# Optimization experiments

Hardware: AMD Instinct MI355X
Metric: run time of the kernel (lower is better)

## Reference

```python
import jax, jax.numpy as jnp
import numpy as np

N, K, D = 32768, 8192, 64

def setup_inputs() -> dict:
    key = jax.random.key(0)
    kx, kc = jax.random.split(key)
    x = jax.random.normal(kx, (N, D), dtype=jnp.float32)
    codebook = jax.random.normal(kc, (K, D), dtype=jnp.float32)
    return {"x": x, "codebook": codebook}

def reference(x, codebook):
    # Faithful to: argmin(((codebook[None] - x[:, None])**2).sum(-1), -1)
    # Computed via the expanded squared distance to avoid the [N, K, D]
    # constant per row and does not affect argmin, but we include it so the
    # distance matrix matches the original math exactly.
    x_sq = jnp.sum(x * x, axis=-1, keepdims=True)          # [N, 1]
    c_sq = jnp.sum(codebook * codebook, axis=-1)           # [K]
    cross = jnp.einsum('nd,kd->nk', x, codebook)           # [N, K]
    dists = x_sq - 2.0 * cross + c_sq[None, :]             # [N, K]
    return jnp.argmin(dists, axis=-1)                      # [N] int32
```

## Files before the change

kernel.cpp:

```cpp
#include <hip/hip_runtime.h>
#include <math.h>


typedef __attribute__((ext_vector_type(8)))  _Float16 h8v;
typedef __attribute__((ext_vector_type(16))) float f16v;
typedef __attribute__((ext_vector_type(4)))  float f4v;

constexpr int NROWS = 32768;
constexpr int KC    = 8192;
constexpr int DD    = 64;
constexpr int TPB   = 256;
constexpr int BROWS = 64;
constexpr int BTILE = 64;
constexpr int NT    = KC / BTILE;
constexpr int TILE_HALFS = BTILE * DD * 2;

__device__ __forceinline__ void split2h(float v, _Float16& h1, _Float16& h2) {
  const float av = fabsf(v);
  _Float16 a = (_Float16)v;
  if (av < 6.1035156e-5f) a = (_Float16)0.f;
  h1 = a;
  h2 = (_Float16)((v - (float)a) * 4096.f);
}

__device__ __forceinline__ void gload_lds16(const void* g, void* l) {
  __builtin_amdgcn_global_load_lds(
      (const __attribute__((address_space(1))) void*)g,
      (__attribute__((address_space(3))) void*)l, 16, 0, 0);
}

__global__ void vq_pre_kernel(const float* __restrict__ x,
                              const float* __restrict__ cb,
                              _Float16* __restrict__ bSwz,
                              float* __restrict__ csq,
                              float* __restrict__ xsq) {
  const int bid = blockIdx.x, tid = threadIdx.x;
  if (bid < KC / TPB) {
    const int code = bid * TPB + tid;
    const float* cp = cb + (size_t)code * DD;
    float v[DD];
#pragma unroll
    for (int d = 0; d < DD; d += 4) {
      const float4 g = *(const float4*)(cp + d);
      v[d] = g.x; v[d + 1] = g.y; v[d + 2] = g.z; v[d + 3] = g.w;
    }
    float s = 0.f;
#pragma unroll
    for (int d = 0; d < DD; ++d) s = fmaf(v[d], v[d], s);
    csq[code] = s;
    _Float16 p1[DD], p2[DD];
#pragma unroll
    for (int d = 0; d < DD; ++d) split2h(v[d], p1[d], p2[d]);
    const int g = code >> 5, l = code & 31;
    _Float16* base = bSwz + (size_t)g * 4096;
#pragma unroll
    for (int p = 0; p < 2; ++p) {
      const _Float16* pl = p ? p2 : p1;
#pragma unroll
      for (int kc4 = 0; kc4 < 4; ++kc4)
#pragma unroll
        for (int h = 0; h < 2; ++h) {
          h8v wv;
#pragma unroll
          for (int j = 0; j < 8; ++j) wv[j] = pl[kc4 * 16 + h * 8 + j];
          *(h8v*)(base + (p * 4 + kc4) * 512 + (h * 32 + l) * 8) = wv;
        }
    }
  } else {
    const int n = (bid - KC / TPB) * TPB + tid;
    const float* xp = x + (size_t)n * DD;
    float s = 0.f;
#pragma unroll
    for (int d = 0; d < DD; ++d) s = fmaf(xp[d], xp[d], s);
    xsq[n] = s;
  }
}

__global__ __launch_bounds__(TPB, 2)
void vq_mfma_kernel(const float* __restrict__ x, const _Float16* __restrict__ bSwz,
                    const float* __restrict__ csq_g, const float* __restrict__ xsq_g,
                    int* __restrict__ out) {
  __shared__ alignas(16) _Float16 ldsA[2][BROWS][DD];
  __shared__ alignas(16) _Float16 ldsB[2][TILE_HALFS];
  __shared__ alignas(16) float ldsXsq[BROWS];
  __shared__ unsigned long long ldsRed[BROWS][2];

  const int tid  = threadIdx.x;
  const int lane = tid & 63;
  const int w    = tid >> 6;
  const int s    = w & 1;
  const int ch   = w >> 1;
  const int half = lane >> 5;
  const int col  = lane & 31;
  const int blockRow = blockIdx.x * BROWS;

  {
    const _Float16* src0 = bSwz + (size_t)(w * 4) * 512 + lane * 8;
#pragma unroll
    for (int j = 0; j < 4; ++j)
      gload_lds16(src0 + j * 512, &ldsB[0][(w * 4 + j) * 512]);
  }
  {
    const int row = tid >> 2, dseg = (tid & 3) * 16;
    const float* xp = x + (size_t)(blockRow + row) * DD + dseg;
    float v[16];
#pragma unroll
    for (int d = 0; d < 16; d += 4) {
      const float4 g = *(const float4*)(xp + d);
      v[d] = g.x; v[d + 1] = g.y; v[d + 2] = g.z; v[d + 3] = g.w;
    }
    _Float16 qa[16], qb[16];
#pragma unroll
    for (int e = 0; e < 16; ++e) split2h(v[e], qa[e], qb[e]);
#pragma unroll
    for (int h2 = 0; h2 < 2; ++h2) {
      h8v a, b;
#pragma unroll
      for (int j = 0; j < 8; ++j) { a[j] = qa[h2 * 8 + j]; b[j] = qb[h2 * 8 + j]; }
      *(h8v*)&ldsA[0][row][dseg + h2 * 8] = a;
      *(h8v*)&ldsA[1][row][dseg + h2 * 8] = b;
    }
  }
  if (tid < BROWS) ldsXsq[tid] = xsq_g[blockRow + tid];
  __syncthreads();

  h8v afr[2][4];
#pragma unroll
  for (int p = 0; p < 2; ++p)
#pragma unroll
    for (int kc4 = 0; kc4 < 4; ++kc4)
      afr[p][kc4] = *(const h8v*)&ldsA[p][s * 32 + col][kc4 * 16 + half * 8];

  float xq[16];
  {
    const float* xb = &ldsXsq[s * 32 + 4 * half];
#pragma unroll
    for (int g8 = 0; g8 < 4; ++g8) {
      const f4v t4 = *(const f4v*)(xb + g8 * 8);
      xq[g8 * 4] = t4[0]; xq[g8 * 4 + 1] = t4[1];
      xq[g8 * 4 + 2] = t4[2]; xq[g8 * 4 + 3] = t4[3];
    }
  }

  float bestD[16];
  unsigned bestC[16];
#pragma unroll
  for (int i = 0; i < 16; ++i) { bestD[i] = INFINITY; bestC[i] = 0u; }

  for (int t = 0; t < NT; ++t) {
    const int buf = t & 1;
    if (t + 1 < NT) {
      const _Float16* src =
          bSwz + (size_t)(t + 1) * TILE_HALFS + (size_t)(w * 4) * 512 + lane * 8;
#pragma unroll
      for (int j = 0; j < 4; ++j)
        gload_lds16(src + j * 512, &ldsB[buf ^ 1][(w * 4 + j) * 512]);
    }
    const float cs = csq_g[t * BTILE + ch * 32 + col];

    h8v bfr[2][4];
#pragma unroll
    for (int p = 0; p < 2; ++p)
#pragma unroll
      for (int kc4 = 0; kc4 < 4; ++kc4)
        bfr[p][kc4] = *(const h8v*)
            &ldsB[buf][(ch * 8 + p * 4 + kc4) * 512 + lane * 8];

    f16v accA  = {0.f,0.f,0.f,0.f,0.f,0.f,0.f,0.f,0.f,0.f,0.f,0.f,0.f,0.f,0.f,0.f};
    f16v accB1 = {0.f,0.f,0.f,0.f,0.f,0.f,0.f,0.f,0.f,0.f,0.f,0.f,0.f,0.f,0.f,0.f};
    f16v accB2 = {0.f,0.f,0.f,0.f,0.f,0.f,0.f,0.f,0.f,0.f,0.f,0.f,0.f,0.f,0.f,0.f};
#pragma unroll
    for (int kc4 = 0; kc4 < 4; ++kc4) {
      accA  = __builtin_amdgcn_mfma_f32_32x32x16_f16(afr[0][kc4], bfr[0][kc4], accA,  0, 0, 0);
      accB1 = __builtin_amdgcn_mfma_f32_32x32x16_f16(afr[0][kc4], bfr[1][kc4], accB1, 0, 0, 0);
      accB2 = __builtin_amdgcn_mfma_f32_32x32x16_f16(afr[1][kc4], bfr[0][kc4], accB2, 0, 0, 0);
    }

    const unsigned code = (unsigned)(t * BTILE + ch * 32 + col);
#pragma unroll
    for (int i = 0; i < 16; ++i) {
      const float acc = fmaf(accB1[i] + accB2[i], 2.44140625e-4f, accA[i]);
      const float dist = fmaf(-2.f, acc, xq[i]) + cs;
      if (dist < bestD[i]) { bestD[i] = dist; bestC[i] = code; }
    }
    __syncthreads();
  }

  unsigned long long key[16];
#pragma unroll
  for (int i = 0; i < 16; ++i)
    key[i] = ((unsigned long long)__float_as_uint(bestD[i]) << 32) | bestC[i];
#pragma unroll
  for (int i = 0; i < 16; ++i) {
#pragma unroll
    for (int m = 1; m < 32; m <<= 1) {
      const unsigned long long o = __shfl_xor(key[i], m, 64);
      if (o < key[i]) key[i] = o;
    }
  }
  if (col == 0) {
#pragma unroll
    for (int i = 0; i < 16; ++i) {
      const int row = s * 32 + (i & 3) + 8 * (i >> 2) + 4 * half;
      ldsRed[row][ch] = key[i];
    }
  }
  __syncthreads();
  if (tid < BROWS) {
    const unsigned long long a = ldsRed[tid][0];
    const unsigned long long b = ldsRed[tid][1];
    out[blockRow + tid] = (int)(unsigned)((a < b ? a : b) & 0xFFFFFFFFull);
  }
}

extern "C" void kernel_launch(void* const* d_in, const int* in_sizes, int n_in,
                              void* d_out, int out_size, void* d_ws, size_t ws_size,
                              hipStream_t stream) {
  const float* x  = (const float*)d_in[0];
  const float* cb = (const float*)d_in[1];
  int* out = (int*)d_out;

  _Float16* bSwz = (_Float16*)d_ws;
  float* csq_g = (float*)((char*)d_ws + (size_t)KC * DD * 2 * 2);
  float* xsq_g = csq_g + KC;

  vq_pre_kernel<<<dim3(KC / TPB + NROWS / TPB), dim3(TPB), 0, stream>>>(
      x, cb, bSwz, csq_g, xsq_g);
  vq_mfma_kernel<<<dim3(NROWS / BROWS), dim3(TPB), 0, stream>>>(
      x, bSwz, csq_g, xsq_g, out);
}
```

Measured before the change: 192.6 us.

## Triple-buffer codebook tiles with software-pipelined MFMA epilogue and fused x-norm

The main loop moves to a three-buffer LDS ring that prefetches two tiles ahead. Codebook norms are staged into LDS alongside each tile, and synchronisation uses a raw waitcnt+barrier that allows outstanding loads to remain in flight. Each tile's argmin epilogue is deferred so it overlaps the next tile's MFMAs, and the two correction MFMAs share one accumulator. The x-norm computation moves from the pre-kernel into the main kernel, shrinking the pre-kernel, at the cost of more LDS, more registers, and fragile hand-counted vmcnt values.

```diff
diff --git a/kernel.cpp b/kernel.cpp
--- a/kernel.cpp
+++ b/kernel.cpp
@@ -14,6 +14,7 @@
 constexpr int BTILE = 64;
 constexpr int NT    = KC / BTILE;
 constexpr int TILE_HALFS = BTILE * DD * 2;
+constexpr int BUF_HALFS  = TILE_HALFS + 512;
 
 __device__ __forceinline__ void split2h(float v, _Float16& h1, _Float16& h2) {
   const float av = fabsf(v);
@@ -28,60 +29,96 @@
       (const __attribute__((address_space(1))) void*)g,
       (__attribute__((address_space(3))) void*)l, 16, 0, 0);
 }
-
-__global__ void vq_pre_kernel(const float* __restrict__ x,
-                              const float* __restrict__ cb,
+__device__ __forceinline__ void gload_lds4(const void* g, void* l) {
+  __builtin_amdgcn_global_load_lds(
+      (const __attribute__((address_space(1))) void*)g,
+      (__attribute__((address_space(3))) void*)l, 4, 0, 0);
+}
+
+__global__ void vq_pre_kernel(const float* __restrict__ cb,
                               _Float16* __restrict__ bSwz,
-                              float* __restrict__ csq,
-                              float* __restrict__ xsq) {
+                              float* __restrict__ csq) {
   const int bid = blockIdx.x, tid = threadIdx.x;
-  if (bid < KC / TPB) {
-    const int code = bid * TPB + tid;
-    const float* cp = cb + (size_t)code * DD;
-    float v[DD];
-#pragma unroll
-    for (int d = 0; d < DD; d += 4) {
-      const float4 g = *(const float4*)(cp + d);
-      v[d] = g.x; v[d + 1] = g.y; v[d + 2] = g.z; v[d + 3] = g.w;
-    }
-    float s = 0.f;
-#pragma unroll
-    for (int d = 0; d < DD; ++d) s = fmaf(v[d], v[d], s);
-    csq[code] = s;
-    _Float16 p1[DD], p2[DD];
-#pragma unroll
-    for (int d = 0; d < DD; ++d) split2h(v[d], p1[d], p2[d]);
-    const int g = code >> 5, l = code & 31;
-    _Float16* base = bSwz + (size_t)g * 4096;
-#pragma unroll
-    for (int p = 0; p < 2; ++p) {
-      const _Float16* pl = p ? p2 : p1;
-#pragma unroll
-      for (int kc4 = 0; kc4 < 4; ++kc4)
-#pragma unroll
-        for (int h = 0; h < 2; ++h) {
-          h8v wv;
-#pragma unroll
-          for (int j = 0; j < 8; ++j) wv[j] = pl[kc4 * 16 + h * 8 + j];
-          *(h8v*)(base + (p * 4 + kc4) * 512 + (h * 32 + l) * 8) = wv;
-        }
-    }
-  } else {
-    const int n = (bid - KC / TPB) * TPB + tid;
-    const float* xp = x + (size_t)n * DD;
-    float s = 0.f;
-#pragma unroll
-    for (int d = 0; d < DD; ++d) s = fmaf(xp[d], xp[d], s);
-    xsq[n] = s;
-  }
-}
+  const int code = bid * TPB + tid;
+  const float* cp = cb + (size_t)code * DD;
+  float v[DD];
+#pragma unroll
+  for (int d = 0; d < DD; d += 4) {
+    const float4 g = *(const float4*)(cp + d);
+    v[d] = g.x; v[d + 1] = g.y; v[d + 2] = g.z; v[d + 3] = g.w;
+  }
+  float s = 0.f;
+#pragma unroll
+  for (int d = 0; d < DD; ++d) s = fmaf(v[d], v[d], s);
+  csq[code] = s;
+  _Float16 p1[DD], p2[DD];
+#pragma unroll
+  for (int d = 0; d < DD; ++d) split2h(v[d], p1[d], p2[d]);
+  const int g = code >> 5, l = code & 31;
+  _Float16* base = bSwz + (size_t)g * 4096;
+#pragma unroll
+  for (int p = 0; p < 2; ++p) {
+    const _Float16* pl = p ? p2 : p1;
+#pragma unroll
+    for (int kc4 = 0; kc4 < 4; ++kc4)
+#pragma unroll
+      for (int h = 0; h < 2; ++h) {
+        h8v wv;
+#pragma unroll
+        for (int j = 0; j < 8; ++j) wv[j] = pl[kc4 * 16 + h * 8 + j];
+        *(h8v*)(base + (p * 4 + kc4) * 512 + (h * 32 + l) * 8) = wv;
+      }
+  }
+}
+
+#define TILE_BODY(T, BUFC, PFB, AA, AB, CS, CODE, PA, PB, PCS, PCODE, DOEPI, DOISSUE, WN) \
+  {                                                                                       \
+    _Float16* bp = ldsBf + (BUFC) * BUF_HALFS;                                            \
+    h8v b0[4], b1[4];                                                                     \
+    {                                                                                     \
+      const _Float16* rb = bp + (ch * 8) * 512 + lane * 8;                                \
+      _Pragma("unroll")                                                                   \
+      for (int kc = 0; kc < 4; ++kc) {                                                    \
+        b0[kc] = *(const h8v*)(rb + kc * 512);                                            \
+        b1[kc] = *(const h8v*)(rb + (4 + kc) * 512);                                      \
+      }                                                                                   \
+    }                                                                                     \
+    CS = ((const float*)(bp + TILE_HALFS))[w * 64 + wcode];                               \
+    CODE = (unsigned)((T) * 64) + wcode;                                                  \
+    if (DOISSUE) {                                                                        \
+      const _Float16* gs = bSwz + (size_t)((T) + 2) * TILE_HALFS + (w * 4) * 512 + lane * 8; \
+      _Float16* ld = ldsBf + (PFB) * BUF_HALFS;                                           \
+      _Pragma("unroll")                                                                   \
+      for (int j = 0; j < 4; ++j)                                                         \
+        gload_lds16(gs + j * 512, ld + (w * 4 + j) * 512);                                \
+      gload_lds4(csq_g + ((T) + 2) * 64 + lane, (float*)(ld + TILE_HALFS) + w * 64);      \
+    }                                                                                     \
+    AA = __builtin_amdgcn_mfma_f32_32x32x16_f16(afr[0][0], b0[0], Zacc, 0, 0, 0);         \
+    AB = __builtin_amdgcn_mfma_f32_32x32x16_f16(afr[0][0], b1[0], Zacc, 0, 0, 0);         \
+    _Pragma("unroll")                                                                     \
+    for (int kc = 1; kc < 4; ++kc) {                                                      \
+      AA = __builtin_amdgcn_mfma_f32_32x32x16_f16(afr[0][kc], b0[kc], AA, 0, 0, 0);       \
+      AB = __builtin_amdgcn_mfma_f32_32x32x16_f16(afr[0][kc], b1[kc], AB, 0, 0, 0);       \
+    }                                                                                     \
+    _Pragma("unroll")                                                                     \
+    for (int kc = 0; kc < 4; ++kc)                                                        \
+      AB = __builtin_amdgcn_mfma_f32_32x32x16_f16(afr[1][kc], b0[kc], AB, 0, 0, 0);       \
+    if (DOEPI) {                                                                          \
+      _Pragma("unroll")                                                                   \
+      for (int i = 0; i < 16; ++i) {                                                      \
+        const float a_ = fmaf(PB[i], 2.44140625e-4f, PA[i]);                              \
+        const float d_ = fmaf(-2.f, a_, xq[i]) + PCS;                                     \
+        if (d_ < bestD[i]) { bestD[i] = d_; bestC[i] = PCODE; }                           \
+      }                                                                                   \
+    }                                                                                     \
+    asm volatile("s_waitcnt vmcnt(" #WN ") lgkmcnt(0)\n\ts_barrier" ::: "memory");        \
+  }
 
 __global__ __launch_bounds__(TPB, 2)
 void vq_mfma_kernel(const float* __restrict__ x, const _Float16* __restrict__ bSwz,
-                    const float* __restrict__ csq_g, const float* __restrict__ xsq_g,
-                    int* __restrict__ out) {
+                    const float* __restrict__ csq_g, int* __restrict__ out) {
   __shared__ alignas(16) _Float16 ldsA[2][BROWS][DD];
-  __shared__ alignas(16) _Float16 ldsB[2][TILE_HALFS];
+  __shared__ alignas(16) _Float16 ldsBf[3 * BUF_HALFS];
   __shared__ alignas(16) float ldsXsq[BROWS];
   __shared__ unsigned long long ldsRed[BROWS][2];
 
@@ -92,13 +129,17 @@
   const int ch   = w >> 1;
   const int half = lane >> 5;
   const int col  = lane & 31;
+  const int wcode = ch * 32 + col;
   const int blockRow = blockIdx.x * BROWS;
 
-  {
-    const _Float16* src0 = bSwz + (size_t)(w * 4) * 512 + lane * 8;
+#pragma unroll
+  for (int tt = 0; tt < 2; ++tt) {
+    const _Float16* gs = bSwz + (size_t)tt * TILE_HALFS + (w * 4) * 512 + lane * 8;
+    _Float16* ld = ldsBf + tt * BUF_HALFS;
 #pragma unroll
     for (int j = 0; j < 4; ++j)
-      gload_lds16(src0 + j * 512, &ldsB[0][(w * 4 + j) * 512]);
+      gload_lds16(gs + j * 512, ld + (w * 4 + j) * 512);
+    gload_lds4(csq_g + tt * 64 + lane, (float*)(ld + TILE_HALFS) + w * 64);
   }
   {
     const int row = tid >> 2, dseg = (tid & 3) * 16;
@@ -109,6 +150,12 @@
       const float4 g = *(const float4*)(xp + d);
       v[d] = g.x; v[d + 1] = g.y; v[d + 2] = g.z; v[d + 3] = g.w;
     }
+    float p = 0.f;
+#pragma unroll
+    for (int e = 0; e < 16; ++e) p = fmaf(v[e], v[e], p);
+    p += __shfl_xor(p, 1, 64);
+    p += __shfl_xor(p, 2, 64);
+    if ((tid & 3) == 0) ldsXsq[row] = p;
     _Float16 qa[16], qb[16];
 #pragma unroll
     for (int e = 0; e < 16; ++e) split2h(v[e], qa[e], qb[e]);
@@ -121,7 +168,6 @@
       *(h8v*)&ldsA[1][row][dseg + h2 * 8] = b;
     }
   }
-  if (tid < BROWS) ldsXsq[tid] = xsq_g[blockRow + tid];
   __syncthreads();
 
   h8v afr[2][4];
@@ -147,43 +193,32 @@
 #pragma unroll
   for (int i = 0; i < 16; ++i) { bestD[i] = INFINITY; bestC[i] = 0u; }
 
-  for (int t = 0; t < NT; ++t) {
-    const int buf = t & 1;
-    if (t + 1 < NT) {
-      const _Float16* src =
-          bSwz + (size_t)(t + 1) * TILE_HALFS + (size_t)(w * 4) * 512 + lane * 8;
-#pragma unroll
-      for (int j = 0; j < 4; ++j)
-        gload_lds16(src + j * 512, &ldsB[buf ^ 1][(w * 4 + j) * 512]);
-    }
-    const float cs = csq_g[t * BTILE + ch * 32 + col];
-
-    h8v bfr[2][4];
-#pragma unroll
-    for (int p = 0; p < 2; ++p)
-#pragma unroll
-      for (int kc4 = 0; kc4 < 4; ++kc4)
-        bfr[p][kc4] = *(const h8v*)
-            &ldsB[buf][(ch * 8 + p * 4 + kc4) * 512 + lane * 8];
-
-    f16v accA  = {0.f,0.f,0.f,0.f,0.f,0.f,0.f,0.f,0.f,0.f,0.f,0.f,0.f,0.f,0.f,0.f};
-    f16v accB1 = {0.f,0.f,0.f,0.f,0.f,0.f,0.f,0.f,0.f,0.f,0.f,0.f,0.f,0.f,0.f,0.f};
-    f16v accB2 = {0.f,0.f,0.f,0.f,0.f,0.f,0.f,0.f,0.f,0.f,0.f,0.f,0.f,0.f,0.f,0.f};
-#pragma unroll
-    for (int kc4 = 0; kc4 < 4; ++kc4) {
-      accA  = __builtin_amdgcn_mfma_f32_32x32x16_f16(afr[0][kc4], bfr[0][kc4], accA,  0, 0, 0);
-      accB1 = __builtin_amdgcn_mfma_f32_32x32x16_f16(afr[0][kc4], bfr[1][kc4], accB1, 0, 0, 0);
-      accB2 = __builtin_amdgcn_mfma_f32_32x32x16_f16(afr[1][kc4], bfr[0][kc4], accB2, 0, 0, 0);
-    }
-
-    const unsigned code = (unsigned)(t * BTILE + ch * 32 + col);
-#pragma unroll
-    for (int i = 0; i < 16; ++i) {
-      const float acc = fmaf(accB1[i] + accB2[i], 2.44140625e-4f, accA[i]);
-      const float dist = fmaf(-2.f, acc, xq[i]) + cs;
-      if (dist < bestD[i]) { bestD[i] = dist; bestC[i] = code; }
-    }
-    __syncthreads();
+  const f16v Zacc = {0.f,0.f,0.f,0.f,0.f,0.f,0.f,0.f,0.f,0.f,0.f,0.f,0.f,0.f,0.f,0.f};
+  f16v aA0 = Zacc, aB0 = Zacc, aA1 = Zacc, aB1 = Zacc;
+  float cs0 = 0.f, cs1 = 0.f;
+  unsigned code0 = 0u, code1 = 0u;
+
+  TILE_BODY(0, 0, 2, aA0, aB0, cs0, code0, aA1, aB1, cs1, code1, false, true, 5);
+  TILE_BODY(1, 1, 0, aA1, aB1, cs1, code1, aA0, aB0, cs0, code0, true,  true, 5);
+  for (int t = 2; t < 122; t += 6) {
+    TILE_BODY(t,     2, 1, aA0, aB0, cs0, code0, aA1, aB1, cs1, code1, true, true, 5);
+    TILE_BODY(t + 1, 0, 2, aA1, aB1, cs1, code1, aA0, aB0, cs0, code0, true, true, 5);
+    TILE_BODY(t + 2, 1, 0, aA0, aB0, cs0, code0, aA1, aB1, cs1, code1, true, true, 5);
+    TILE_BODY(t + 3, 2, 1, aA1, aB1, cs1, code1, aA0, aB0, cs0, code0, true, true, 5);
+    TILE_BODY(t + 4, 0, 2, aA0, aB0, cs0, code0, aA1, aB1, cs1, code1, true, true, 5);
+    TILE_BODY(t + 5, 1, 0, aA1, aB1, cs1, code1, aA0, aB0, cs0, code0, true, true, 5);
+  }
+  TILE_BODY(122, 2, 1, aA0, aB0, cs0, code0, aA1, aB1, cs1, code1, true, true,  5);
+  TILE_BODY(123, 0, 2, aA1, aB1, cs1, code1, aA0, aB0, cs0, code0, true, true,  5);
+  TILE_BODY(124, 1, 0, aA0, aB0, cs0, code0, aA1, aB1, cs1, code1, true, true,  5);
+  TILE_BODY(125, 2, 1, aA1, aB1, cs1, code1, aA0, aB0, cs0, code0, true, true,  5);
+  TILE_BODY(126, 0, 2, aA0, aB0, cs0, code0, aA1, aB1, cs1, code1, true, false, 0);
+  TILE_BODY(127, 1, 0, aA1, aB1, cs1, code1, aA0, aB0, cs0, code0, true, false, 0);
+#pragma unroll
+  for (int i = 0; i < 16; ++i) {
+    const float a_ = fmaf(aB1[i], 2.44140625e-4f, aA1[i]);
+    const float d_ = fmaf(-2.f, a_, xq[i]) + cs1;
+    if (d_ < bestD[i]) { bestD[i] = d_; bestC[i] = code1; }
   }
 
   unsigned long long key[16];
@@ -222,10 +257,8 @@
 
   _Float16* bSwz = (_Float16*)d_ws;
   float* csq_g = (float*)((char*)d_ws + (size_t)KC * DD * 2 * 2);
-  float* xsq_g = csq_g + KC;
-
-  vq_pre_kernel<<<dim3(KC / TPB + NROWS / TPB), dim3(TPB), 0, stream>>>(
-      x, cb, bSwz, csq_g, xsq_g);
+
+  vq_pre_kernel<<<dim3(KC / TPB), dim3(TPB), 0, stream>>>(cb, bSwz, csq_g);
   vq_mfma_kernel<<<dim3(NROWS / BROWS), dim3(TPB), 0, stream>>>(
-      x, bSwz, csq_g, xsq_g, out);
-}
+      x, bSwz, csq_g, out);
+}
```

New measurement: 178.5 us. -7.3%, faster.
